# Optimization experiments

Measured on AMD Instinct MI355X. Metric: run time of the kernel, lower is better.

## Reference

```python
import jax, jax.numpy as jnp
import numpy as np

NUM_WAVELETS = 64      # W
NUM_OUT_CH = 32        # W' (one 2-layer MLP per output channel)
HIDDEN_DIM = 128       # H


def setup_inputs() -> dict:
    key = jax.random.key(0)
    k_x, k_w1, k_b1, k_w2, k_b2 = jax.random.split(key, 5)
    N, C, W, H, O = 4096, 32, NUM_WAVELETS, HIDDEN_DIM, NUM_OUT_CH
    # torch nn.Linear default init: U(-1/sqrt(fan_in), 1/sqrt(fan_in))
    lim1 = 1.0 / np.sqrt(W)
    lim2 = 1.0 / np.sqrt(H)
    return {
        "scalar_inputs": jax.random.normal(k_x, (N, C, W), dtype=jnp.float32),
        # Stacked weights of the O independent MLPs:
        "W1": jax.random.uniform(k_w1, (O, H, W), jnp.float32, -lim1, lim1),
        "b1": jax.random.uniform(k_b1, (O, H), jnp.float32, -lim1, lim1),
        "W2": jax.random.uniform(k_w2, (O, H), jnp.float32, -lim2, lim2),  # Linear(H->1) weight per MLP
        "b2": jax.random.uniform(k_b2, (O,), jnp.float32, -lim2, lim2),
    }


def reference(scalar_inputs, W1, b1, W2, b2):
    # scalar_inputs: [N, C, W]; W1: [O, H, W]; b1: [O, H]; W2: [O, H]; b2: [O]
    N, C, W = scalar_inputs.shape
    x = scalar_inputs.reshape(N * C, W)                      # [NC, W]
    # Batched first Linear over all O MLPs at once (replaces the per-MLP loop)
    h = jax.nn.silu(jnp.einsum("nw,ohw->noh", x, W1) + b1)   # [NC, O, H]
    out = jnp.einsum("noh,oh->no", h, W2) + b2               # [NC, O]
    return out.reshape(N, C, -1)                             # [N, C, O]
```

## Files before the change

kernel.cpp:

```cpp
#include <hip/hip_runtime.h>

#define NC    131072
#define WDIM  64
#define ODIM  32
#define HDIM  128
#define LOG2E 1.4426950408889634f
#define LN2   0.6931471805599453f

typedef __attribute__((ext_vector_type(8))) short bf16x8;
typedef __attribute__((ext_vector_type(4))) float f32x4;
typedef __attribute__((ext_vector_type(4))) float flt4;
typedef __attribute__((ext_vector_type(2))) float f32x2;

__device__ __forceinline__ short f2bf(float f) {
    union { float f; unsigned u; } v; v.f = f;
    unsigned r = (v.u + 0x7FFFu + ((v.u >> 16) & 1u)) >> 16;
    return (short)r;
}

__global__ void prep_kernel(const float* __restrict__ W1, const float* __restrict__ b1,
                            const float* __restrict__ w2, short* __restrict__ w1f,
                            float* __restrict__ b1w2) {
    if (blockIdx.x < 128) {
        int tid  = blockIdx.x * 256 + threadIdx.x;
        int lane = tid & 63;
        int frag = (tid >> 6) & 15;
        int o    = tid >> 10;
        int t    = frag >> 1;
        int k2   = frag & 1;
        const float* src = W1 + ((size_t)(o * HDIM + t * 16 + (lane & 15)) * WDIM
                                 + k2 * 32 + (lane >> 4) * 8);
        bf16x8 v;
        #pragma unroll
        for (int i = 0; i < 8; ++i) v[i] = f2bf(src[i] * -LOG2E);
        *reinterpret_cast<bf16x8*>(w1f + (size_t)tid * 8) = v;
    } else {
        int idx = (blockIdx.x - 128) * 256 + threadIdx.x;
        int o = idx >> 8, j = idx & 255;
        b1w2[idx] = (j < 128) ? b1[o * HDIM + j] * -LOG2E
                              : w2[o * HDIM + (j - 128)] * -LN2;
    }
}

__device__ __forceinline__ void async16(void* lds_dst, const void* g_src) {
    __builtin_amdgcn_global_load_lds(
        (const __attribute__((address_space(1))) unsigned int*)g_src,
        (__attribute__((address_space(3))) unsigned int*)lds_dst,
        16, 0, 0);
}

#define BUFSH 8704

__global__ __launch_bounds__(256, 4)
void swr_main(const float* __restrict__ x, const short* __restrict__ w1f,
              const float* __restrict__ b1w2, const float* __restrict__ b2,
              float* __restrict__ out)
{
    __shared__ short w1lds[2 * BUFSH];
    const int tid  = threadIdx.x;
    const int lane = tid & 63;
    const int wid  = tid >> 6;
    const int col  = lane & 15;
    const int kq   = lane >> 4;
    const size_t rowbase = (size_t)blockIdx.x * 128 + (size_t)wid * 32;

    bf16x8 xf[2][2];
    #pragma unroll
    for (int s = 0; s < 2; ++s) {
        #pragma unroll
        for (int k2 = 0; k2 < 2; ++k2) {
            const float* p = x + (rowbase + s * 16 + col) * WDIM + k2 * 32 + kq * 8;
            flt4 lo = *reinterpret_cast<const flt4*>(p);
            flt4 hi = *reinterpret_cast<const flt4*>(p + 4);
            bf16x8 a;
            a[0] = f2bf(lo[0]); a[1] = f2bf(lo[1]); a[2] = f2bf(lo[2]); a[3] = f2bf(lo[3]);
            a[4] = f2bf(hi[0]); a[5] = f2bf(hi[1]); a[6] = f2bf(hi[2]); a[7] = f2bf(hi[3]);
            xf[s][k2] = a;
        }
    }

    #pragma unroll
    for (int f = 0; f < 4; ++f) {
        int frag = wid * 4 + f;
        async16(&w1lds[frag * 512], w1f + frag * 512 + lane * 8);
    }
    if (wid == 0)
        async16(&w1lds[8192], b1w2 + lane * 4);
    __syncthreads();

    float* op0 = out + (rowbase + col) * ODIM;
    float* op1 = out + (rowbase + 16 + col) * ODIM;
    float pu0 = 0.f, pu1 = 0.f;

    #pragma unroll 1
    for (int o = 0; o < ODIM; ++o) {
        const short* cur = &w1lds[(o & 1) * BUFSH];

        if (o > 0 && lane < 16) { op0[o - 1] = pu0; op1[o - 1] = pu1; }

        if (o + 1 < ODIM) {
            const short* g = w1f + (size_t)(o + 1) * 8192;
            short* nb = &w1lds[((o + 1) & 1) * BUFSH];
            #pragma unroll
            for (int f = 0; f < 4; ++f) {
                int frag = wid * 4 + f;
                async16(nb + frag * 512, g + frag * 512 + lane * 8);
            }
            if (wid == 0)
                async16(nb + 8192, b1w2 + (size_t)(o + 1) * 256 + lane * 4);
        }
        const float b2o = b2[o];
        const flt4* bwl = reinterpret_cast<const flt4*>(cur + 8192);

        f32x2 part[2][2];
        #pragma unroll
        for (int s = 0; s < 2; ++s)
            #pragma unroll
            for (int p = 0; p < 2; ++p) part[s][p] = (f32x2){0.f, 0.f};

        #pragma unroll
        for (int t = 0; t < 8; ++t) {
            flt4 b1c = bwl[t * 4 + kq];
            flt4 w2c = bwl[32 + t * 4 + kq];
            bf16x8 f0 = *reinterpret_cast<const bf16x8*>(cur + (t * 2 + 0) * 512 + lane * 8);
            bf16x8 f1 = *reinterpret_cast<const bf16x8*>(cur + (t * 2 + 1) * 512 + lane * 8);
            #pragma unroll
            for (int s = 0; s < 2; ++s) {
                f32x4 acc = __builtin_amdgcn_mfma_f32_16x16x32_bf16(
                                f0, xf[s][0], (f32x4){b1c[0], b1c[1], b1c[2], b1c[3]}, 0, 0, 0);
                acc = __builtin_amdgcn_mfma_f32_16x16x32_bf16(f1, xf[s][1], acc, 0, 0, 0);
                #pragma unroll
                for (int p = 0; p < 2; ++p) {
                    f32x2 m  = { acc[2 * p], acc[2 * p + 1] };
                    f32x2 wp = { w2c[2 * p], w2c[2 * p + 1] };
                    f32x2 mw = m * wp;
                    f32x2 e  = { __builtin_amdgcn_exp2f(m.x),
                                 __builtin_amdgcn_exp2f(m.y) };
                    f32x2 d  = e + (f32x2){1.f, 1.f};
                    f32x2 sg = { __builtin_amdgcn_rcpf(d.x),
                                 __builtin_amdgcn_rcpf(d.y) };
                    part[s][p] = __builtin_elementwise_fma(mw, sg, part[s][p]);
                }
            }
        }

        {
            f32x2 u2 = part[0][0] + part[0][1];
            float u = u2.x + u2.y;
            u += __shfl_xor(u, 16);
            u += __shfl_xor(u, 32);
            pu0 = u + b2o;
        }
        {
            f32x2 u2 = part[1][0] + part[1][1];
            float u = u2.x + u2.y;
            u += __shfl_xor(u, 16);
            u += __shfl_xor(u, 32);
            pu1 = u + b2o;
        }
        __syncthreads();
    }
    if (lane < 16) { op0[ODIM - 1] = pu0; op1[ODIM - 1] = pu1; }
}

extern "C" void kernel_launch(void* const* d_in, const int* in_sizes, int n_in,
                              void* d_out, int out_size, void* d_ws, size_t ws_size,
                              hipStream_t stream)
{
    const float* x  = (const float*)d_in[0];
    const float* W1 = (const float*)d_in[1];
    const float* b1 = (const float*)d_in[2];
    const float* w2 = (const float*)d_in[3];
    const float* b2 = (const float*)d_in[4];
    float* out = (float*)d_out;
    short* w1f  = (short*)d_ws;
    float* b1w2 = (float*)((char*)d_ws + 512 * 1024);

    hipLaunchKernelGGL(prep_kernel, dim3(160), dim3(256), 0, stream,
                       W1, b1, w2, w1f, b1w2);
    hipLaunchKernelGGL(swr_main, dim3(NC / 128), dim3(256), 0, stream,
                       x, w1f, b1w2, b2, out);
}
```

Baseline: 211.3 us.

## Split output channels across block pairs and double rows per wave

Each block now handles 256 rows (64 per wave, four 16-row MFMA subtiles) but only half of the output channels, with adjacent block pairs splitting the 32 MLPs. Each LDS weight fragment is reused across twice as many rows, and each block runs half as many loop iterations, so there are fewer barriers and async refills per unit of work. The grid size is unchanged. The cost is that every x row is loaded and converted twice (once per half), and each wave holds more live registers for xf, part and the accumulators, which may reduce occupancy under launch_bounds(256,4).

```diff
diff --git a/kernel.cpp b/kernel.cpp
--- a/kernel.cpp
+++ b/kernel.cpp
@@ -50,6 +50,7 @@
 }
 
 #define BUFSH 8704
+#define OHALF 16
 
 __global__ __launch_bounds__(256, 4)
 void swr_main(const float* __restrict__ x, const short* __restrict__ w1f,
@@ -62,11 +63,14 @@
     const int wid  = tid >> 6;
     const int col  = lane & 15;
     const int kq   = lane >> 4;
-    const size_t rowbase = (size_t)blockIdx.x * 128 + (size_t)wid * 32;
+    const int oh   = blockIdx.x & 1;
+    const int rb   = blockIdx.x >> 1;
+    const int obase = oh * OHALF;
+    const size_t rowbase = (size_t)rb * 256 + (size_t)wid * 64;
 
-    bf16x8 xf[2][2];
+    bf16x8 xf[4][2];
     #pragma unroll
-    for (int s = 0; s < 2; ++s) {
+    for (int s = 0; s < 4; ++s) {
         #pragma unroll
         for (int k2 = 0; k2 < 2; ++k2) {
             const float* p = x + (rowbase + s * 16 + col) * WDIM + k2 * 32 + kq * 8;
@@ -82,24 +86,29 @@
     #pragma unroll
     for (int f = 0; f < 4; ++f) {
         int frag = wid * 4 + f;
-        async16(&w1lds[frag * 512], w1f + frag * 512 + lane * 8);
+        async16(&w1lds[frag * 512], w1f + (size_t)obase * 8192 + frag * 512 + lane * 8);
     }
     if (wid == 0)
-        async16(&w1lds[8192], b1w2 + lane * 4);
+        async16(&w1lds[8192], b1w2 + (size_t)obase * 256 + lane * 4);
     __syncthreads();
 
-    float* op0 = out + (rowbase + col) * ODIM;
-    float* op1 = out + (rowbase + 16 + col) * ODIM;
-    float pu0 = 0.f, pu1 = 0.f;
+    float* op[4];
+    #pragma unroll
+    for (int s = 0; s < 4; ++s) op[s] = out + (rowbase + s * 16 + col) * ODIM;
+    float pu[4] = {0.f, 0.f, 0.f, 0.f};
 
     #pragma unroll 1
-    for (int o = 0; o < ODIM; ++o) {
+    for (int o = 0; o < OHALF; ++o) {
+        const int oabs = obase + o;
         const short* cur = &w1lds[(o & 1) * BUFSH];
 
-        if (o > 0 && lane < 16) { op0[o - 1] = pu0; op1[o - 1] = pu1; }
+        if (o > 0 && lane < 16) {
+            #pragma unroll
+            for (int s = 0; s < 4; ++s) op[s][oabs - 1] = pu[s];
+        }
 
-        if (o + 1 < ODIM) {
-            const short* g = w1f + (size_t)(o + 1) * 8192;
+        if (o + 1 < OHALF) {
+            const short* g = w1f + (size_t)(oabs + 1) * 8192;
             short* nb = &w1lds[((o + 1) & 1) * BUFSH];
             #pragma unroll
             for (int f = 0; f < 4; ++f) {
@@ -107,14 +116,14 @@
                 async16(nb + frag * 512, g + frag * 512 + lane * 8);
             }
             if (wid == 0)
-                async16(nb + 8192, b1w2 + (size_t)(o + 1) * 256 + lane * 4);
+                async16(nb + 8192, b1w2 + (size_t)(oabs + 1) * 256 + lane * 4);
         }
-        const float b2o = b2[o];
+        const float b2o = b2[oabs];
         const flt4* bwl = reinterpret_cast<const flt4*>(cur + 8192);
 
-        f32x2 part[2][2];
+        f32x2 part[4][2];
         #pragma unroll
-        for (int s = 0; s < 2; ++s)
+        for (int s = 0; s < 4; ++s)
             #pragma unroll
             for (int p = 0; p < 2; ++p) part[s][p] = (f32x2){0.f, 0.f};
 
@@ -125,7 +134,7 @@
             bf16x8 f0 = *reinterpret_cast<const bf16x8*>(cur + (t * 2 + 0) * 512 + lane * 8);
             bf16x8 f1 = *reinterpret_cast<const bf16x8*>(cur + (t * 2 + 1) * 512 + lane * 8);
             #pragma unroll
-            for (int s = 0; s < 2; ++s) {
+            for (int s = 0; s < 4; ++s) {
                 f32x4 acc = __builtin_amdgcn_mfma_f32_16x16x32_bf16(
                                 f0, xf[s][0], (f32x4){b1c[0], b1c[1], b1c[2], b1c[3]}, 0, 0, 0);
                 acc = __builtin_amdgcn_mfma_f32_16x16x32_bf16(f1, xf[s][1], acc, 0, 0, 0);
@@ -144,23 +153,20 @@
             }
         }
 
-        {
-            f32x2 u2 = part[0][0] + part[0][1];
+        #pragma unroll
+        for (int s = 0; s < 4; ++s) {
+            f32x2 u2 = part[s][0] + part[s][1];
             float u = u2.x + u2.y;
             u += __shfl_xor(u, 16);
             u += __shfl_xor(u, 32);
-            pu0 = u + b2o;
-        }
-        {
-            f32x2 u2 = part[1][0] + part[1][1];
-            float u = u2.x + u2.y;
-            u += __shfl_xor(u, 16);
-            u += __shfl_xor(u, 32);
-            pu1 = u + b2o;
+            pu[s] = u + b2o;
         }
         __syncthreads();
     }
-    if (lane < 16) { op0[ODIM - 1] = pu0; op1[ODIM - 1] = pu1; }
+    if (lane < 16) {
+        #pragma unroll
+        for (int s = 0; s < 4; ++s) op[s][obase + OHALF - 1] = pu[s];
+    }
 }
 
 extern "C" void kernel_launch(void* const* d_in, const int* in_sizes, int n_in,
```

After: 207.9 us. Within noise of the previous version (-1.6%).

## Split output channels across blocks and batch sigmoid reciprocals

Applied to the files above, without the earlier changes.

The main kernel now launches 512-thread blocks covering 256 rows each, and splits the 32 output MLPs into two halves handled by different blocks. Each wave still owns 32 rows but loops over only 16 output channels, with weight fragment staging spread across 8 waves. Separately, the four sigmoid reciprocals per MFMA tile are replaced by one reciprocal of their product plus extra multiplies, to cut transcendental-unit pressure. In exchange, the input rows are loaded and converted twice (once per half). The product of denominators can overflow for large pre-activations, and the aggressive launch bounds may constrain registers.

```diff
diff --git a/kernel.cpp b/kernel.cpp
--- a/kernel.cpp
+++ b/kernel.cpp
@@ -50,8 +50,9 @@
 }
 
 #define BUFSH 8704
+#define OHALF 16
 
-__global__ __launch_bounds__(256, 4)
+__global__ __launch_bounds__(512, 8)
 void swr_main(const float* __restrict__ x, const short* __restrict__ w1f,
               const float* __restrict__ b1w2, const float* __restrict__ b2,
               float* __restrict__ out)
@@ -62,7 +63,10 @@
     const int wid  = tid >> 6;
     const int col  = lane & 15;
     const int kq   = lane >> 4;
-    const size_t rowbase = (size_t)blockIdx.x * 128 + (size_t)wid * 32;
+    const int oh   = blockIdx.x >> 9;
+    const int rb   = blockIdx.x & 511;
+    const int obase = oh * OHALF;
+    const size_t rowbase = (size_t)rb * 256 + (size_t)wid * 32;
 
     bf16x8 xf[2][2];
     #pragma unroll
@@ -80,12 +84,12 @@
     }
 
     #pragma unroll
-    for (int f = 0; f < 4; ++f) {
-        int frag = wid * 4 + f;
-        async16(&w1lds[frag * 512], w1f + frag * 512 + lane * 8);
+    for (int f = 0; f < 2; ++f) {
+        int frag = wid * 2 + f;
+        async16(&w1lds[frag * 512], w1f + (size_t)obase * 8192 + frag * 512 + lane * 8);
     }
     if (wid == 0)
-        async16(&w1lds[8192], b1w2 + lane * 4);
+        async16(&w1lds[8192], b1w2 + (size_t)obase * 256 + lane * 4);
     __syncthreads();
 
     float* op0 = out + (rowbase + col) * ODIM;
@@ -93,23 +97,24 @@
     float pu0 = 0.f, pu1 = 0.f;
 
     #pragma unroll 1
-    for (int o = 0; o < ODIM; ++o) {
+    for (int o = 0; o < OHALF; ++o) {
+        const int oabs = obase + o;
         const short* cur = &w1lds[(o & 1) * BUFSH];
 
-        if (o > 0 && lane < 16) { op0[o - 1] = pu0; op1[o - 1] = pu1; }
+        if (o > 0 && lane < 16) { op0[oabs - 1] = pu0; op1[oabs - 1] = pu1; }
 
-        if (o + 1 < ODIM) {
-            const short* g = w1f + (size_t)(o + 1) * 8192;
+        if (o + 1 < OHALF) {
+            const short* g = w1f + (size_t)(oabs + 1) * 8192;
             short* nb = &w1lds[((o + 1) & 1) * BUFSH];
             #pragma unroll
-            for (int f = 0; f < 4; ++f) {
-                int frag = wid * 4 + f;
+            for (int f = 0; f < 2; ++f) {
+                int frag = wid * 2 + f;
                 async16(nb + frag * 512, g + frag * 512 + lane * 8);
             }
             if (wid == 0)
-                async16(nb + 8192, b1w2 + (size_t)(o + 1) * 256 + lane * 4);
+                async16(nb + 8192, b1w2 + (size_t)(oabs + 1) * 256 + lane * 4);
         }
-        const float b2o = b2[o];
+        const float b2o = b2[oabs];
         const flt4* bwl = reinterpret_cast<const flt4*>(cur + 8192);
 
         f32x2 part[2][2];
@@ -129,18 +134,25 @@
                 f32x4 acc = __builtin_amdgcn_mfma_f32_16x16x32_bf16(
                                 f0, xf[s][0], (f32x4){b1c[0], b1c[1], b1c[2], b1c[3]}, 0, 0, 0);
                 acc = __builtin_amdgcn_mfma_f32_16x16x32_bf16(f1, xf[s][1], acc, 0, 0, 0);
-                #pragma unroll
-                for (int p = 0; p < 2; ++p) {
-                    f32x2 m  = { acc[2 * p], acc[2 * p + 1] };
-                    f32x2 wp = { w2c[2 * p], w2c[2 * p + 1] };
-                    f32x2 mw = m * wp;
-                    f32x2 e  = { __builtin_amdgcn_exp2f(m.x),
-                                 __builtin_amdgcn_exp2f(m.y) };
-                    f32x2 d  = e + (f32x2){1.f, 1.f};
-                    f32x2 sg = { __builtin_amdgcn_rcpf(d.x),
-                                 __builtin_amdgcn_rcpf(d.y) };
-                    part[s][p] = __builtin_elementwise_fma(mw, sg, part[s][p]);
-                }
+                f32x2 mA  = { acc[0], acc[1] };
+                f32x2 mB  = { acc[2], acc[3] };
+                f32x2 mwA = mA * (f32x2){ w2c[0], w2c[1] };
+                f32x2 mwB = mB * (f32x2){ w2c[2], w2c[3] };
+                f32x2 eA  = { __builtin_amdgcn_exp2f(mA.x),
+                              __builtin_amdgcn_exp2f(mA.y) };
+                f32x2 eB  = { __builtin_amdgcn_exp2f(mB.x),
+                              __builtin_amdgcn_exp2f(mB.y) };
+                f32x2 dA  = eA + (f32x2){1.f, 1.f};
+                f32x2 dB  = eB + (f32x2){1.f, 1.f};
+                float qA  = dA.x * dA.y;
+                float qB  = dB.x * dB.y;
+                float R   = __builtin_amdgcn_rcpf(qA * qB);
+                float iqA = R * qB;
+                float iqB = R * qA;
+                f32x2 sA  = { iqA * dA.y, iqA * dA.x };
+                f32x2 sB  = { iqB * dB.y, iqB * dB.x };
+                part[s][0] = __builtin_elementwise_fma(mwA, sA, part[s][0]);
+                part[s][1] = __builtin_elementwise_fma(mwB, sB, part[s][1]);
             }
         }
 
@@ -160,7 +172,7 @@
         }
         __syncthreads();
     }
-    if (lane < 16) { op0[ODIM - 1] = pu0; op1[ODIM - 1] = pu1; }
+    if (lane < 16) { op0[obase + OHALF - 1] = pu0; op1[obase + OHALF - 1] = pu1; }
 }
 
 extern "C" void kernel_launch(void* const* d_in, const int* in_sizes, int n_in,
@@ -178,6 +190,6 @@
 
     hipLaunchKernelGGL(prep_kernel, dim3(160), dim3(256), 0, stream,
                        W1, b1, w2, w1f, b1w2);
-    hipLaunchKernelGGL(swr_main, dim3(NC / 128), dim3(256), 0, stream,
+    hipLaunchKernelGGL(swr_main, dim3(1024), dim3(512), 0, stream,
                        x, w1f, b1w2, b2, out);
 }
```

After: 226.3 us. 7.1% more time.
